# Optimization experiments

Measured on AMD Instinct MI355X. Metric: run time of the kernel, lower is better.

## Reference

```python
import jax, jax.numpy as jnp
import numpy as np

B, S, F, H = 512, 1024, 16, 64
BN_EPS = 1e-3  # Keras BatchNormalization default epsilon


def setup_inputs() -> dict:
    key = jax.random.key(0)
    ks = jax.random.split(key, 8)
    scale = 0.1
    return {
        "inputs": jax.random.normal(ks[0], (B, S, F), dtype=jnp.float32),
        "gru_kernel": jax.random.normal(ks[1], (F - 1, 3 * H), dtype=jnp.float32) * scale,
        "gru_rec_kernel": jax.random.normal(ks[2], (H, 3 * H), dtype=jnp.float32) * scale,
        "gru_bias": jax.random.normal(ks[3], (2, 3 * H), dtype=jnp.float32) * scale,
        "w1": jax.random.normal(ks[4], (H, 64), dtype=jnp.float32) * scale,
        "b1": jnp.zeros((64,), dtype=jnp.float32),
        "bn_gamma": jnp.ones((64,), dtype=jnp.float32),
        "bn_beta": jnp.zeros((64,), dtype=jnp.float32),
        "bn_mean": jnp.zeros((64,), dtype=jnp.float32),
        "bn_var": jnp.ones((64,), dtype=jnp.float32),
        "w2": jax.random.normal(ks[5], (64, 1), dtype=jnp.float32) * scale,
        "b2": jnp.zeros((1,), dtype=jnp.float32),
        "T": jax.random.normal(ks[6], (1,), dtype=jnp.float32),
    }


def _gru_scan(x, kernel, rec_kernel, bias):
    # Keras GRU, reset_after=True, gate order (z, r, h). x: [B, S, Fin]
    b_i, b_r = bias[0], bias[1]  # input bias, recurrent bias, each [3H]
    # Precompute input projections for all timesteps: [B, S, 3H]
    x_proj = jnp.einsum("bsf,fg->bsg", x, kernel) + b_i
    h0 = jnp.zeros((x.shape[0], rec_kernel.shape[0]), dtype=x.dtype)

    def step(h, xp):
        rp = h @ rec_kernel + b_r  # [B, 3H]
        xz, xr, xh = jnp.split(xp, 3, axis=-1)
        rz, rr, rh = jnp.split(rp, 3, axis=-1)
        z = jax.nn.sigmoid(xz + rz)
        r = jax.nn.sigmoid(xr + rr)
        hh = jnp.tanh(xh + r * rh)
        h_new = z * h + (1.0 - z) * hh
        return h_new, None

    h_final, _ = jax.lax.scan(step, h0, jnp.swapaxes(x_proj, 0, 1))
    return h_final  # [B, H]


def reference(inputs, gru_kernel, gru_rec_kernel, gru_bias, w1, b1,
              bn_gamma, bn_beta, bn_mean, bn_var, w2, b2, T):
    x = inputs[:, :, :-1]                 # [B, S, F-1]
    delta_x_shifted = inputs[:, :, -1]    # [B, S]
    state = _gru_scan(x, gru_kernel, gru_rec_kernel, gru_bias)  # [B, H]
    # T * delta tiled to H then mean over time == T * mean_t(delta), broadcast over H
    delta_effect = T[0] * jnp.mean(delta_x_shifted, axis=1, keepdims=True)  # [B, 1]
    state = state + delta_effect  # broadcasts over H
    h = jax.nn.relu(state @ w1 + b1)
    # Dropout identity at inference; BatchNorm uses moving statistics
    h = (h - bn_mean) * jax.lax.rsqrt(bn_var + BN_EPS) * bn_gamma + bn_beta
    out = h @ w2 + b2  # [B, 1]
    return out
```

## Files before the change

### kernel.cpp

```cpp
#include <hip/hip_runtime.h>
#include <hip/hip_bf16.h>


#define KEEP(x) asm volatile("" : "+v"(x))

typedef _Float16 f16x2 __attribute__((ext_vector_type(2)));
union H2U { unsigned int u; f16x2 h; };

#if defined(__has_builtin)
#  if __has_builtin(__builtin_amdgcn_fdot2)
#    define HAS_FDOT2 1
#  endif
#endif
#ifndef HAS_FDOT2
#  define HAS_FDOT2 0
#endif

static __device__ __forceinline__ float dot2acc(unsigned int hraw, unsigned int wraw, float acc) {
    H2U a, b; a.u = hraw; b.u = wraw;
#if HAS_FDOT2
    return __builtin_amdgcn_fdot2(a.h, b.h, acc, false);
#else
    return fmaf((float)a.h.x, (float)b.h.x, fmaf((float)a.h.y, (float)b.h.y, acc));
#endif
}

template<bool BF16>
struct IO {
    static __device__ __forceinline__ float ld(const void* p, int i) {
        if constexpr (BF16) {
            unsigned short u = ((const unsigned short*)p)[i];
            union { unsigned int ui; float f; } c; c.ui = (unsigned int)u << 16;
            return c.f;
        } else {
            return ((const float*)p)[i];
        }
    }
    static __device__ __forceinline__ void st(void* p, int i, float v) {
        if constexpr (BF16) ((__hip_bfloat16*)p)[i] = __float2bfloat16(v);
        else ((float*)p)[i] = v;
    }
    static __device__ __forceinline__ float4 ld4(const void* p, int i) {
        if constexpr (BF16) {
            const ushort4 u = ((const ushort4*)p)[i >> 2];
            union { unsigned int ui; float f; } a, b, c, d;
            a.ui = (unsigned int)u.x << 16; b.ui = (unsigned int)u.y << 16;
            c.ui = (unsigned int)u.z << 16; d.ui = (unsigned int)u.w << 16;
            return make_float4(a.f, b.f, c.f, d.f);
        } else {
            return ((const float4*)p)[i >> 2];
        }
    }
};

__global__ void detect_dtype_kernel(const void* rkbuf, int* flag) {
    const float* f = (const float*)rkbuf;
    int ok = 0;
    for (int i = 0; i < 64; ++i) {
        float a = fabsf(f[i]);
        ok += (a > 1e-5f && a < 2.0f) ? 1 : 0;
    }
    *flag = (ok >= 48) ? 1 : 0;
}

template<bool BF16>
__global__ __launch_bounds__(128, 1)
void gru_pc_kernel(const void* __restrict__ inp, const void* __restrict__ gk,
                   const void* __restrict__ rk,  const void* __restrict__ gb,
                   const void* __restrict__ w1,  const void* __restrict__ b1v,
                   const void* __restrict__ gam, const void* __restrict__ bet,
                   const void* __restrict__ muv, const void* __restrict__ vav,
                   const void* __restrict__ w2,  const void* __restrict__ bb2,
                   const void* __restrict__ Tp,  const int* __restrict__ mode,
                   void* __restrict__ out)
{
    const int want = BF16 ? 0 : 1;
    if (*mode != want) return;

    const int b   = blockIdx.x;
    const int tid = threadIdx.x;
    const int w   = tid >> 6;
    const int l   = tid & 63;

    __shared__ __align__(16) float xp[2][16][64][4];
    __shared__ __align__(16) float xs[16][16];
    __shared__ __align__(16) _Float16 hsf[64];
    __shared__ __align__(16) float sred[64];
    __shared__ float dsh;

    using io = IO<BF16>;
    const int xbase = b * 16384;

    if (w == 1) {
        float kz[15], kr[15], kh[15];
#pragma unroll
        for (int c = 0; c < 15; ++c) {
            kz[c] = io::ld(gk, c*192 + l);
            kr[c] = io::ld(gk, c*192 + 64 + l);
            kh[c] = io::ld(gk, c*192 + 128 + l);
            KEEP(kz[c]); KEEP(kr[c]); KEEP(kh[c]);
        }
        const float bz  = io::ld(gb, l)      + io::ld(gb, 192 + l);
        const float br  = io::ld(gb, 64 + l) + io::ld(gb, 192 + 64 + l);
        const float bax = io::ld(gb, 128 + l);
        float dsum = 0.0f;

        auto produce = [&](int buf) {
#pragma unroll 1
            for (int s2 = 0; s2 < 16; ++s2) {
                const float4* xr = (const float4*)&xs[s2][0];
                const float4 x0 = xr[0], x1 = xr[1], x2 = xr[2], x3 = xr[3];
                float az = bz, ar = br, ax = bax;
                az=fmaf(x0.x,kz[0],az);  ar=fmaf(x0.x,kr[0],ar);  ax=fmaf(x0.x,kh[0],ax);
                az=fmaf(x0.y,kz[1],az);  ar=fmaf(x0.y,kr[1],ar);  ax=fmaf(x0.y,kh[1],ax);
                az=fmaf(x0.z,kz[2],az);  ar=fmaf(x0.z,kr[2],ar);  ax=fmaf(x0.z,kh[2],ax);
                az=fmaf(x0.w,kz[3],az);  ar=fmaf(x0.w,kr[3],ar);  ax=fmaf(x0.w,kh[3],ax);
                az=fmaf(x1.x,kz[4],az);  ar=fmaf(x1.x,kr[4],ar);  ax=fmaf(x1.x,kh[4],ax);
                az=fmaf(x1.y,kz[5],az);  ar=fmaf(x1.y,kr[5],ar);  ax=fmaf(x1.y,kh[5],ax);
                az=fmaf(x1.z,kz[6],az);  ar=fmaf(x1.z,kr[6],ar);  ax=fmaf(x1.z,kh[6],ax);
                az=fmaf(x1.w,kz[7],az);  ar=fmaf(x1.w,kr[7],ar);  ax=fmaf(x1.w,kh[7],ax);
                az=fmaf(x2.x,kz[8],az);  ar=fmaf(x2.x,kr[8],ar);  ax=fmaf(x2.x,kh[8],ax);
                az=fmaf(x2.y,kz[9],az);  ar=fmaf(x2.y,kr[9],ar);  ax=fmaf(x2.y,kh[9],ax);
                az=fmaf(x2.z,kz[10],az); ar=fmaf(x2.z,kr[10],ar); ax=fmaf(x2.z,kh[10],ax);
                az=fmaf(x2.w,kz[11],az); ar=fmaf(x2.w,kr[11],ar); ax=fmaf(x2.w,kh[11],ax);
                az=fmaf(x3.x,kz[12],az); ar=fmaf(x3.x,kr[12],ar); ax=fmaf(x3.x,kh[12],ax);
                az=fmaf(x3.y,kz[13],az); ar=fmaf(x3.y,kr[13],ar); ax=fmaf(x3.y,kh[13],ax);
                az=fmaf(x3.z,kz[14],az); ar=fmaf(x3.z,kr[14],ar); ax=fmaf(x3.z,kh[14],ax);
                dsum += x3.w;
                *(float4*)&xp[buf][s2][l][0] = make_float4(az, ar, ax, 0.0f);
            }
        };

        {
            float4 v = io::ld4(inp, xbase + 4*l);
            ((float4*)xs)[l] = v;
            produce(0);
        }
        __syncthreads();

#pragma unroll 1
        for (int t = 0; t < 64; ++t) {
            if (t < 63) {
                float4 v = io::ld4(inp, xbase + (t + 1)*256 + 4*l);
                ((float4*)xs)[l] = v;
                produce((t + 1) & 1);
            } else if (l == 0) {
                dsh = dsum;
            }
            __syncthreads();
        }
        return;
    }

    unsigned int wzp[32], wrp[32], whp[32];
#pragma unroll
    for (int p = 0; p < 32; ++p) {
        H2U z, r, hh;
        z.h  = f16x2{(_Float16)io::ld(rk, (2*p)*192 + l),
                     (_Float16)io::ld(rk, (2*p+1)*192 + l)};
        r.h  = f16x2{(_Float16)io::ld(rk, (2*p)*192 + 64 + l),
                     (_Float16)io::ld(rk, (2*p+1)*192 + 64 + l)};
        hh.h = f16x2{(_Float16)io::ld(rk, (2*p)*192 + 128 + l),
                     (_Float16)io::ld(rk, (2*p+1)*192 + 128 + l)};
        wzp[p] = z.u; wrp[p] = r.u; whp[p] = hh.u;
        KEEP(wzp[p]); KEEP(wrp[p]); KEEP(whp[p]);
    }
    const float bah = io::ld(gb, 192 + 128 + l);

    hsf[l] = (_Float16)0.0f;
    float h = 0.0f;
    __syncthreads();

#pragma unroll 1
    for (int t = 0; t < 64; ++t) {
        const float (*xpt)[64][4] = xp[t & 1];
#pragma unroll 1
        for (int s2 = 0; s2 < 16; ++s2) {
            const float4 xpv = *(const float4*)&xpt[s2][l][0];
            const uint4* hp = (const uint4*)hsf;
            float az = xpv.x, ar = xpv.y;
            const float ax = xpv.z;
            float ah = bah;
            float az1 = 0.0f, ar1 = 0.0f, ah1 = 0.0f;
#pragma unroll
            for (int i = 0; i < 4; ++i) {
                const uint4 d = hp[i];
                az = dot2acc(d.x, wzp[4*i+0], az); ar = dot2acc(d.x, wrp[4*i+0], ar); ah = dot2acc(d.x, whp[4*i+0], ah);
                az = dot2acc(d.y, wzp[4*i+1], az); ar = dot2acc(d.y, wrp[4*i+1], ar); ah = dot2acc(d.y, whp[4*i+1], ah);
                az = dot2acc(d.z, wzp[4*i+2], az); ar = dot2acc(d.z, wrp[4*i+2], ar); ah = dot2acc(d.z, whp[4*i+2], ah);
                az = dot2acc(d.w, wzp[4*i+3], az); ar = dot2acc(d.w, wrp[4*i+3], ar); ah = dot2acc(d.w, whp[4*i+3], ah);
            }
#pragma unroll
            for (int i = 4; i < 8; ++i) {
                const uint4 d = hp[i];
                az1 = dot2acc(d.x, wzp[4*i+0], az1); ar1 = dot2acc(d.x, wrp[4*i+0], ar1); ah1 = dot2acc(d.x, whp[4*i+0], ah1);
                az1 = dot2acc(d.y, wzp[4*i+1], az1); ar1 = dot2acc(d.y, wrp[4*i+1], ar1); ah1 = dot2acc(d.y, whp[4*i+1], ah1);
                az1 = dot2acc(d.z, wzp[4*i+2], az1); ar1 = dot2acc(d.z, wrp[4*i+2], ar1); ah1 = dot2acc(d.z, whp[4*i+2], ah1);
                az1 = dot2acc(d.w, wzp[4*i+3], az1); ar1 = dot2acc(d.w, wrp[4*i+3], ar1); ah1 = dot2acc(d.w, whp[4*i+3], ah1);
            }
            az += az1; ar += ar1; ah += ah1;

            const float z   = __builtin_amdgcn_rcpf(1.0f + __expf(-az));
            const float r   = __builtin_amdgcn_rcpf(1.0f + __expf(-ar));
            const float pre = fmaf(r, ah, ax);
            const float e2  = __expf(2.0f * pre);
            const float th  = 1.0f - 2.0f * __builtin_amdgcn_rcpf(e2 + 1.0f);
            h = fmaf(z, h - th, th);

            hsf[l] = (_Float16)h;
        }
        __syncthreads();
    }

    const float T0 = io::ld(Tp, 0);
    const float state = fmaf(T0 * (1.0f / 1024.0f), dsh, h);
    sred[l] = state;

    const int j = l;
    float acc = io::ld(b1v, j);
#pragma unroll
    for (int k = 0; k < 64; ++k)
        acc = fmaf(sred[k], io::ld(w1, k*64 + j), acc);
    acc = fmaxf(acc, 0.0f);
    const float inv = rsqrtf(io::ld(vav, j) + 0.001f);
    acc = fmaf((acc - io::ld(muv, j)) * inv, io::ld(gam, j), io::ld(bet, j));

    float v = acc * io::ld(w2, j);
#pragma unroll
    for (int off = 32; off > 0; off >>= 1)
        v += __shfl_down(v, off);
    if (j == 0) io::st(out, b, v + io::ld(bb2, 0));
}

extern "C" void kernel_launch(void* const* d_in, const int* in_sizes, int n_in,
                              void* d_out, int out_size, void* d_ws, size_t ws_size,
                              hipStream_t stream)
{
    const void* inp = d_in[0];
    const void* gk  = d_in[1];
    const void* rk  = d_in[2];
    const void* gb  = d_in[3];
    const void* w1  = d_in[4];
    const void* b1v = d_in[5];
    const void* gam = d_in[6];
    const void* bet = d_in[7];
    const void* muv = d_in[8];
    const void* vav = d_in[9];
    const void* w2  = d_in[10];
    const void* bb2 = d_in[11];
    const void* Tp  = d_in[12];

    int* flag = (int*)d_ws;
    detect_dtype_kernel<<<dim3(1), dim3(1), 0, stream>>>(rk, flag);
    gru_pc_kernel<true ><<<dim3(512), dim3(128), 0, stream>>>(
        inp, gk, rk, gb, w1, b1v, gam, bet, muv, vav, w2, bb2, Tp, flag, d_out);
    gru_pc_kernel<false><<<dim3(512), dim3(128), 0, stream>>>(
        inp, gk, rk, gb, w1, b1v, gam, bet, muv, vav, w2, bb2, Tp, flag, d_out);
}
```

Measured before the change: 460.7 us.

## Process two batch rows per block to interleave independent GRU recurrences

Each block now handles two batch elements. The producer wave computes input projections for both, and the recurrent wave alternates steps between the two hidden states, keeping h vectors in registers. The intent is to hide the serial per-step latency of the recurrence (LDS round trip, transcendentals) by overlapping two independent dependency chains. It halves the grid size and increases register pressure, which could reduce parallelism across CUs.

```diff
diff --git a/kernel.cpp b/kernel.cpp
--- a/kernel.cpp
+++ b/kernel.cpp
@@ -65,31 +65,30 @@
 
 template<bool BF16>
 __global__ __launch_bounds__(128, 1)
-void gru_pc_kernel(const void* __restrict__ inp, const void* __restrict__ gk,
-                   const void* __restrict__ rk,  const void* __restrict__ gb,
-                   const void* __restrict__ w1,  const void* __restrict__ b1v,
-                   const void* __restrict__ gam, const void* __restrict__ bet,
-                   const void* __restrict__ muv, const void* __restrict__ vav,
-                   const void* __restrict__ w2,  const void* __restrict__ bb2,
-                   const void* __restrict__ Tp,  const int* __restrict__ mode,
-                   void* __restrict__ out)
+void gru_pc2_kernel(const void* __restrict__ inp, const void* __restrict__ gk,
+                    const void* __restrict__ rk,  const void* __restrict__ gb,
+                    const void* __restrict__ w1,  const void* __restrict__ b1v,
+                    const void* __restrict__ gam, const void* __restrict__ bet,
+                    const void* __restrict__ muv, const void* __restrict__ vav,
+                    const void* __restrict__ w2,  const void* __restrict__ bb2,
+                    const void* __restrict__ Tp,  const int* __restrict__ mode,
+                    void* __restrict__ out)
 {
     const int want = BF16 ? 0 : 1;
     if (*mode != want) return;
 
-    const int b   = blockIdx.x;
+    const int b0  = blockIdx.x * 2;
     const int tid = threadIdx.x;
     const int w   = tid >> 6;
     const int l   = tid & 63;
 
-    __shared__ __align__(16) float xp[2][16][64][4];
-    __shared__ __align__(16) float xs[16][16];
-    __shared__ __align__(16) _Float16 hsf[64];
-    __shared__ __align__(16) float sred[64];
-    __shared__ float dsh;
+    __shared__ __align__(16) float xp[2][2][8][64][4];
+    __shared__ __align__(16) float xs[2][8][16];
+    __shared__ __align__(16) _Float16 hsf[2][64];
+    __shared__ __align__(16) float sred[2][64];
+    __shared__ float dsh[2];
 
     using io = IO<BF16>;
-    const int xbase = b * 16384;
 
     if (w == 1) {
         float kz[15], kr[15], kh[15];
@@ -103,49 +102,47 @@
         const float bz  = io::ld(gb, l)      + io::ld(gb, 192 + l);
         const float br  = io::ld(gb, 64 + l) + io::ld(gb, 192 + 64 + l);
         const float bax = io::ld(gb, 128 + l);
-        float dsum = 0.0f;
-
+        float dsum0 = 0.0f, dsum1 = 0.0f;
+
+        const int bat = l >> 5;
+        const int q   = l & 31;
+
+        auto stage = [&](int t) {
+            float4 v = io::ld4(inp, (b0 + bat)*16384 + t*128 + q*4);
+            *(float4*)&xs[bat][q >> 2][(q & 3) * 4] = v;
+        };
         auto produce = [&](int buf) {
 #pragma unroll 1
-            for (int s2 = 0; s2 < 16; ++s2) {
-                const float4* xr = (const float4*)&xs[s2][0];
-                const float4 x0 = xr[0], x1 = xr[1], x2 = xr[2], x3 = xr[3];
-                float az = bz, ar = br, ax = bax;
-                az=fmaf(x0.x,kz[0],az);  ar=fmaf(x0.x,kr[0],ar);  ax=fmaf(x0.x,kh[0],ax);
-                az=fmaf(x0.y,kz[1],az);  ar=fmaf(x0.y,kr[1],ar);  ax=fmaf(x0.y,kh[1],ax);
-                az=fmaf(x0.z,kz[2],az);  ar=fmaf(x0.z,kr[2],ar);  ax=fmaf(x0.z,kh[2],ax);
-                az=fmaf(x0.w,kz[3],az);  ar=fmaf(x0.w,kr[3],ar);  ax=fmaf(x0.w,kh[3],ax);
-                az=fmaf(x1.x,kz[4],az);  ar=fmaf(x1.x,kr[4],ar);  ax=fmaf(x1.x,kh[4],ax);
-                az=fmaf(x1.y,kz[5],az);  ar=fmaf(x1.y,kr[5],ar);  ax=fmaf(x1.y,kh[5],ax);
-                az=fmaf(x1.z,kz[6],az);  ar=fmaf(x1.z,kr[6],ar);  ax=fmaf(x1.z,kh[6],ax);
-                az=fmaf(x1.w,kz[7],az);  ar=fmaf(x1.w,kr[7],ar);  ax=fmaf(x1.w,kh[7],ax);
-                az=fmaf(x2.x,kz[8],az);  ar=fmaf(x2.x,kr[8],ar);  ax=fmaf(x2.x,kh[8],ax);
-                az=fmaf(x2.y,kz[9],az);  ar=fmaf(x2.y,kr[9],ar);  ax=fmaf(x2.y,kh[9],ax);
-                az=fmaf(x2.z,kz[10],az); ar=fmaf(x2.z,kr[10],ar); ax=fmaf(x2.z,kh[10],ax);
-                az=fmaf(x2.w,kz[11],az); ar=fmaf(x2.w,kr[11],ar); ax=fmaf(x2.w,kh[11],ax);
-                az=fmaf(x3.x,kz[12],az); ar=fmaf(x3.x,kr[12],ar); ax=fmaf(x3.x,kh[12],ax);
-                az=fmaf(x3.y,kz[13],az); ar=fmaf(x3.y,kr[13],ar); ax=fmaf(x3.y,kh[13],ax);
-                az=fmaf(x3.z,kz[14],az); ar=fmaf(x3.z,kr[14],ar); ax=fmaf(x3.z,kh[14],ax);
-                dsum += x3.w;
-                *(float4*)&xp[buf][s2][l][0] = make_float4(az, ar, ax, 0.0f);
+            for (int ab = 0; ab < 2; ++ab) {
+#pragma unroll 1
+                for (int s2 = 0; s2 < 8; ++s2) {
+                    const float4* xr = (const float4*)&xs[ab][s2][0];
+                    const float4 x0 = xr[0], x1 = xr[1], x2 = xr[2], x3 = xr[3];
+                    const float xc[16] = {x0.x,x0.y,x0.z,x0.w, x1.x,x1.y,x1.z,x1.w,
+                                          x2.x,x2.y,x2.z,x2.w, x3.x,x3.y,x3.z,x3.w};
+                    float az = bz, ar = br, ax = bax;
+#pragma unroll
+                    for (int c = 0; c < 15; ++c) {
+                        az = fmaf(xc[c], kz[c], az);
+                        ar = fmaf(xc[c], kr[c], ar);
+                        ax = fmaf(xc[c], kh[c], ax);
+                    }
+                    if (ab == 0) dsum0 += xc[15]; else dsum1 += xc[15];
+                    *(float4*)&xp[buf][ab][s2][l][0] = make_float4(az, ar, ax, 0.0f);
+                }
             }
         };
 
-        {
-            float4 v = io::ld4(inp, xbase + 4*l);
-            ((float4*)xs)[l] = v;
-            produce(0);
-        }
+        stage(0); produce(0);
         __syncthreads();
 
 #pragma unroll 1
-        for (int t = 0; t < 64; ++t) {
-            if (t < 63) {
-                float4 v = io::ld4(inp, xbase + (t + 1)*256 + 4*l);
-                ((float4*)xs)[l] = v;
+        for (int t = 0; t < 128; ++t) {
+            if (t < 127) {
+                stage(t + 1);
                 produce((t + 1) & 1);
             } else if (l == 0) {
-                dsh = dsum;
+                dsh[0] = dsum0; dsh[1] = dsum1;
             }
             __syncthreads();
         }
@@ -167,69 +164,97 @@
     }
     const float bah = io::ld(gb, 192 + 128 + l);
 
-    hsf[l] = (_Float16)0.0f;
-    float h = 0.0f;
+    uint4 ha[8], hb[8];
+#pragma unroll
+    for (int i = 0; i < 8; ++i) { ha[i] = make_uint4(0,0,0,0); hb[i] = make_uint4(0,0,0,0); }
+    float hA = 0.0f, hB = 0.0f;
+
+    auto step_batch = [&](uint4 (&hr)[8], const float4& xpv, float& h,
+                          _Float16* hbuf) {
+        float az = xpv.x, ar = xpv.y;
+        const float ax = xpv.z;
+        float ah = bah;
+        float az1 = 0.0f, ar1 = 0.0f, ah1 = 0.0f;
+#pragma unroll
+        for (int i = 0; i < 4; ++i) {
+            const uint4 d = hr[i];
+            az = dot2acc(d.x, wzp[4*i+0], az); ar = dot2acc(d.x, wrp[4*i+0], ar); ah = dot2acc(d.x, whp[4*i+0], ah);
+            az = dot2acc(d.y, wzp[4*i+1], az); ar = dot2acc(d.y, wrp[4*i+1], ar); ah = dot2acc(d.y, whp[4*i+1], ah);
+            az = dot2acc(d.z, wzp[4*i+2], az); ar = dot2acc(d.z, wrp[4*i+2], ar); ah = dot2acc(d.z, whp[4*i+2], ah);
+            az = dot2acc(d.w, wzp[4*i+3], az); ar = dot2acc(d.w, wrp[4*i+3], ar); ah = dot2acc(d.w, whp[4*i+3], ah);
+        }
+#pragma unroll
+        for (int i = 4; i < 8; ++i) {
+            const uint4 d = hr[i];
+            az1 = dot2acc(d.x, wzp[4*i+0], az1); ar1 = dot2acc(d.x, wrp[4*i+0], ar1); ah1 = dot2acc(d.x, whp[4*i+0], ah1);
+            az1 = dot2acc(d.y, wzp[4*i+1], az1); ar1 = dot2acc(d.y, wrp[4*i+1], ar1); ah1 = dot2acc(d.y, whp[4*i+1], ah1);
+            az1 = dot2acc(d.z, wzp[4*i+2], az1); ar1 = dot2acc(d.z, wrp[4*i+2], ar1); ah1 = dot2acc(d.z, whp[4*i+2], ah1);
+            az1 = dot2acc(d.w, wzp[4*i+3], az1); ar1 = dot2acc(d.w, wrp[4*i+3], ar1); ah1 = dot2acc(d.w, whp[4*i+3], ah1);
+        }
+        az += az1; ar += ar1; ah += ah1;
+
+        const float z   = __builtin_amdgcn_rcpf(1.0f + __expf(-az));
+        const float r   = __builtin_amdgcn_rcpf(1.0f + __expf(-ar));
+        const float pre = fmaf(r, ah, ax);
+        const float e2  = __expf(2.0f * pre);
+        const float th  = 1.0f - 2.0f * __builtin_amdgcn_rcpf(e2 + 1.0f);
+        h = fmaf(z, h - th, th);
+
+        hbuf[l] = (_Float16)h;
+        const uint4* hp = (const uint4*)hbuf;
+#pragma unroll
+        for (int i = 0; i < 8; ++i) hr[i] = hp[i];
+    };
+
     __syncthreads();
-
-#pragma unroll 1
-    for (int t = 0; t < 64; ++t) {
-        const float (*xpt)[64][4] = xp[t & 1];
-#pragma unroll 1
-        for (int s2 = 0; s2 < 16; ++s2) {
-            const float4 xpv = *(const float4*)&xpt[s2][l][0];
-            const uint4* hp = (const uint4*)hsf;
-            float az = xpv.x, ar = xpv.y;
-            const float ax = xpv.z;
-            float ah = bah;
-            float az1 = 0.0f, ar1 = 0.0f, ah1 = 0.0f;
-#pragma unroll
-            for (int i = 0; i < 4; ++i) {
-                const uint4 d = hp[i];
-                az = dot2acc(d.x, wzp[4*i+0], az); ar = dot2acc(d.x, wrp[4*i+0], ar); ah = dot2acc(d.x, whp[4*i+0], ah);
-                az = dot2acc(d.y, wzp[4*i+1], az); ar = dot2acc(d.y, wrp[4*i+1], ar); ah = dot2acc(d.y, whp[4*i+1], ah);
-                az = dot2acc(d.z, wzp[4*i+2], az); ar = dot2acc(d.z, wrp[4*i+2], ar); ah = dot2acc(d.z, whp[4*i+2], ah);
-                az = dot2acc(d.w, wzp[4*i+3], az); ar = dot2acc(d.w, wrp[4*i+3], ar); ah = dot2acc(d.w, whp[4*i+3], ah);
-            }
-#pragma unroll
-            for (int i = 4; i < 8; ++i) {
-                const uint4 d = hp[i];
-                az1 = dot2acc(d.x, wzp[4*i+0], az1); ar1 = dot2acc(d.x, wrp[4*i+0], ar1); ah1 = dot2acc(d.x, whp[4*i+0], ah1);
-                az1 = dot2acc(d.y, wzp[4*i+1], az1); ar1 = dot2acc(d.y, wrp[4*i+1], ar1); ah1 = dot2acc(d.y, whp[4*i+1], ah1);
-                az1 = dot2acc(d.z, wzp[4*i+2], az1); ar1 = dot2acc(d.z, wrp[4*i+2], ar1); ah1 = dot2acc(d.z, whp[4*i+2], ah1);
-                az1 = dot2acc(d.w, wzp[4*i+3], az1); ar1 = dot2acc(d.w, wrp[4*i+3], ar1); ah1 = dot2acc(d.w, whp[4*i+3], ah1);
-            }
-            az += az1; ar += ar1; ah += ah1;
-
-            const float z   = __builtin_amdgcn_rcpf(1.0f + __expf(-az));
-            const float r   = __builtin_amdgcn_rcpf(1.0f + __expf(-ar));
-            const float pre = fmaf(r, ah, ax);
-            const float e2  = __expf(2.0f * pre);
-            const float th  = 1.0f - 2.0f * __builtin_amdgcn_rcpf(e2 + 1.0f);
-            h = fmaf(z, h - th, th);
-
-            hsf[l] = (_Float16)h;
+    float4 xA = *(const float4*)&xp[0][0][0][l][0];
+    float4 xB = *(const float4*)&xp[0][1][0][l][0];
+
+#pragma unroll 1
+    for (int t = 0; t < 128; ++t) {
+#pragma unroll 1
+        for (int s2 = 0; s2 < 8; ++s2) {
+            step_batch(ha, xA, hA, &hsf[0][0]);
+            if (s2 < 7) xA = *(const float4*)&xp[t & 1][0][s2 + 1][l][0];
+            step_batch(hb, xB, hB, &hsf[1][0]);
+            if (s2 < 7) xB = *(const float4*)&xp[t & 1][1][s2 + 1][l][0];
         }
         __syncthreads();
+        if (t < 127) {
+            xA = *(const float4*)&xp[(t + 1) & 1][0][0][l][0];
+            xB = *(const float4*)&xp[(t + 1) & 1][1][0][l][0];
+        }
     }
 
     const float T0 = io::ld(Tp, 0);
-    const float state = fmaf(T0 * (1.0f / 1024.0f), dsh, h);
-    sred[l] = state;
+    sred[0][l] = fmaf(T0 * (1.0f / 1024.0f), dsh[0], hA);
+    sred[1][l] = fmaf(T0 * (1.0f / 1024.0f), dsh[1], hB);
 
     const int j = l;
-    float acc = io::ld(b1v, j);
-#pragma unroll
-    for (int k = 0; k < 64; ++k)
-        acc = fmaf(sred[k], io::ld(w1, k*64 + j), acc);
-    acc = fmaxf(acc, 0.0f);
+    float accA = io::ld(b1v, j), accB = accA;
+#pragma unroll
+    for (int k = 0; k < 64; ++k) {
+        const float wv = io::ld(w1, k*64 + j);
+        accA = fmaf(sred[0][k], wv, accA);
+        accB = fmaf(sred[1][k], wv, accB);
+    }
     const float inv = rsqrtf(io::ld(vav, j) + 0.001f);
-    acc = fmaf((acc - io::ld(muv, j)) * inv, io::ld(gam, j), io::ld(bet, j));
-
-    float v = acc * io::ld(w2, j);
-#pragma unroll
-    for (int off = 32; off > 0; off >>= 1)
-        v += __shfl_down(v, off);
-    if (j == 0) io::st(out, b, v + io::ld(bb2, 0));
+    const float mu = io::ld(muv, j), ga = io::ld(gam, j), be = io::ld(bet, j);
+    accA = fmaf((fmaxf(accA, 0.0f) - mu) * inv, ga, be);
+    accB = fmaf((fmaxf(accB, 0.0f) - mu) * inv, ga, be);
+
+    const float w2j = io::ld(w2, j);
+    float vA = accA * w2j, vB = accB * w2j;
+#pragma unroll
+    for (int off = 32; off > 0; off >>= 1) {
+        vA += __shfl_down(vA, off);
+        vB += __shfl_down(vB, off);
+    }
+    if (j == 0) {
+        const float b2v = io::ld(bb2, 0);
+        io::st(out, b0,     vA + b2v);
+        io::st(out, b0 + 1, vB + b2v);
+    }
 }
 
 extern "C" void kernel_launch(void* const* d_in, const int* in_sizes, int n_in,
@@ -252,8 +277,8 @@
 
     int* flag = (int*)d_ws;
     detect_dtype_kernel<<<dim3(1), dim3(1), 0, stream>>>(rk, flag);
-    gru_pc_kernel<true ><<<dim3(512), dim3(128), 0, stream>>>(
+    gru_pc2_kernel<true ><<<dim3(256), dim3(128), 0, stream>>>(
         inp, gk, rk, gb, w1, b1v, gam, bet, muv, vav, w2, bb2, Tp, flag, d_out);
-    gru_pc_kernel<false><<<dim3(512), dim3(128), 0, stream>>>(
+    gru_pc2_kernel<false><<<dim3(256), dim3(128), 0, stream>>>(
         inp, gk, rk, gb, w1, b1v, gam, bet, muv, vav, w2, bb2, Tp, flag, d_out);
 }
```

Result: slower. 815.7 us (+77.1%).

## Merge producer wave into single-wave GRU kernel with staged input in LDS

Applied to the files above, without the earlier changes.

Replaces the two-wave producer/consumer scheme with a single 64-thread wave per batch row. The row's inputs are bulk-copied into LDS (in two halves for fp32), and each step computes the input projection inline. The next timestep's x is prefetched from LDS while the recurrent dot products run. Because the block is a single wave, the per-chunk __syncthreads barriers disappear and h is exchanged through LDS without a block barrier. The trade-off is that projection FMAs now sit on the serial critical path of every step, and register pressure rises from holding both weight sets.

```diff
diff --git a/kernel.cpp b/kernel.cpp
--- a/kernel.cpp
+++ b/kernel.cpp
@@ -6,6 +6,7 @@
 
 typedef _Float16 f16x2 __attribute__((ext_vector_type(2)));
 union H2U { unsigned int u; f16x2 h; };
+union FU  { unsigned int u; float f; };
 
 #if defined(__has_builtin)
 #  if __has_builtin(__builtin_amdgcn_fdot2)
@@ -30,7 +31,7 @@
     static __device__ __forceinline__ float ld(const void* p, int i) {
         if constexpr (BF16) {
             unsigned short u = ((const unsigned short*)p)[i];
-            union { unsigned int ui; float f; } c; c.ui = (unsigned int)u << 16;
+            FU c; c.u = (unsigned int)u << 16;
             return c.f;
         } else {
             return ((const float*)p)[i];
@@ -39,17 +40,6 @@
     static __device__ __forceinline__ void st(void* p, int i, float v) {
         if constexpr (BF16) ((__hip_bfloat16*)p)[i] = __float2bfloat16(v);
         else ((float*)p)[i] = v;
-    }
-    static __device__ __forceinline__ float4 ld4(const void* p, int i) {
-        if constexpr (BF16) {
-            const ushort4 u = ((const ushort4*)p)[i >> 2];
-            union { unsigned int ui; float f; } a, b, c, d;
-            a.ui = (unsigned int)u.x << 16; b.ui = (unsigned int)u.y << 16;
-            c.ui = (unsigned int)u.z << 16; d.ui = (unsigned int)u.w << 16;
-            return make_float4(a.f, b.f, c.f, d.f);
-        } else {
-            return ((const float4*)p)[i >> 2];
-        }
     }
 };
 
@@ -64,8 +54,8 @@
 }
 
 template<bool BF16>
-__global__ __launch_bounds__(128, 1)
-void gru_pc_kernel(const void* __restrict__ inp, const void* __restrict__ gk,
+__global__ __launch_bounds__(64, 1)
+void gru_sw_kernel(const void* __restrict__ inp, const void* __restrict__ gk,
                    const void* __restrict__ rk,  const void* __restrict__ gb,
                    const void* __restrict__ w1,  const void* __restrict__ b1v,
                    const void* __restrict__ gam, const void* __restrict__ bet,
@@ -77,79 +67,25 @@
     const int want = BF16 ? 0 : 1;
     if (*mode != want) return;
 
-    const int b   = blockIdx.x;
-    const int tid = threadIdx.x;
-    const int w   = tid >> 6;
-    const int l   = tid & 63;
-
-    __shared__ __align__(16) float xp[2][16][64][4];
-    __shared__ __align__(16) float xs[16][16];
+    const int b = blockIdx.x;
+    const int l = threadIdx.x;
+
+    __shared__ __align__(16) unsigned char xsm[32768];
     __shared__ __align__(16) _Float16 hsf[64];
-    __shared__ __align__(16) float sred[64];
-    __shared__ float dsh;
+    __shared__ __align__(16) float sredf[64];
 
     using io = IO<BF16>;
-    const int xbase = b * 16384;
-
-    if (w == 1) {
-        float kz[15], kr[15], kh[15];
-#pragma unroll
-        for (int c = 0; c < 15; ++c) {
-            kz[c] = io::ld(gk, c*192 + l);
-            kr[c] = io::ld(gk, c*192 + 64 + l);
-            kh[c] = io::ld(gk, c*192 + 128 + l);
-            KEEP(kz[c]); KEEP(kr[c]); KEEP(kh[c]);
-        }
-        const float bz  = io::ld(gb, l)      + io::ld(gb, 192 + l);
-        const float br  = io::ld(gb, 64 + l) + io::ld(gb, 192 + 64 + l);
-        const float bax = io::ld(gb, 128 + l);
-        float dsum = 0.0f;
-
-        auto produce = [&](int buf) {
-#pragma unroll 1
-            for (int s2 = 0; s2 < 16; ++s2) {
-                const float4* xr = (const float4*)&xs[s2][0];
-                const float4 x0 = xr[0], x1 = xr[1], x2 = xr[2], x3 = xr[3];
-                float az = bz, ar = br, ax = bax;
-                az=fmaf(x0.x,kz[0],az);  ar=fmaf(x0.x,kr[0],ar);  ax=fmaf(x0.x,kh[0],ax);
-                az=fmaf(x0.y,kz[1],az);  ar=fmaf(x0.y,kr[1],ar);  ax=fmaf(x0.y,kh[1],ax);
-                az=fmaf(x0.z,kz[2],az);  ar=fmaf(x0.z,kr[2],ar);  ax=fmaf(x0.z,kh[2],ax);
-                az=fmaf(x0.w,kz[3],az);  ar=fmaf(x0.w,kr[3],ar);  ax=fmaf(x0.w,kh[3],ax);
-                az=fmaf(x1.x,kz[4],az);  ar=fmaf(x1.x,kr[4],ar);  ax=fmaf(x1.x,kh[4],ax);
-                az=fmaf(x1.y,kz[5],az);  ar=fmaf(x1.y,kr[5],ar);  ax=fmaf(x1.y,kh[5],ax);
-                az=fmaf(x1.z,kz[6],az);  ar=fmaf(x1.z,kr[6],ar);  ax=fmaf(x1.z,kh[6],ax);
-                az=fmaf(x1.w,kz[7],az);  ar=fmaf(x1.w,kr[7],ar);  ax=fmaf(x1.w,kh[7],ax);
-                az=fmaf(x2.x,kz[8],az);  ar=fmaf(x2.x,kr[8],ar);  ax=fmaf(x2.x,kh[8],ax);
-                az=fmaf(x2.y,kz[9],az);  ar=fmaf(x2.y,kr[9],ar);  ax=fmaf(x2.y,kh[9],ax);
-                az=fmaf(x2.z,kz[10],az); ar=fmaf(x2.z,kr[10],ar); ax=fmaf(x2.z,kh[10],ax);
-                az=fmaf(x2.w,kz[11],az); ar=fmaf(x2.w,kr[11],ar); ax=fmaf(x2.w,kh[11],ax);
-                az=fmaf(x3.x,kz[12],az); ar=fmaf(x3.x,kr[12],ar); ax=fmaf(x3.x,kh[12],ax);
-                az=fmaf(x3.y,kz[13],az); ar=fmaf(x3.y,kr[13],ar); ax=fmaf(x3.y,kh[13],ax);
-                az=fmaf(x3.z,kz[14],az); ar=fmaf(x3.z,kr[14],ar); ax=fmaf(x3.z,kh[14],ax);
-                dsum += x3.w;
-                *(float4*)&xp[buf][s2][l][0] = make_float4(az, ar, ax, 0.0f);
-            }
-        };
-
-        {
-            float4 v = io::ld4(inp, xbase + 4*l);
-            ((float4*)xs)[l] = v;
-            produce(0);
-        }
-        __syncthreads();
-
-#pragma unroll 1
-        for (int t = 0; t < 64; ++t) {
-            if (t < 63) {
-                float4 v = io::ld4(inp, xbase + (t + 1)*256 + 4*l);
-                ((float4*)xs)[l] = v;
-                produce((t + 1) & 1);
-            } else if (l == 0) {
-                dsh = dsum;
-            }
-            __syncthreads();
-        }
-        return;
+    const uint4* gin = (const uint4*)inp;
+    uint4* xv = (uint4*)xsm;
+
+    if constexpr (BF16) {
+#pragma unroll 4
+        for (int i = 0; i < 32; ++i)
+            xv[i*64 + l] = gin[b*2048 + i*64 + l];
+    } else {
+#pragma unroll 4
+        for (int i = 0; i < 32; ++i)
+            xv[i*64 + l] = gin[b*4096 + i*64 + l];
     }
 
     unsigned int wzp[32], wrp[32], whp[32];
@@ -165,62 +101,142 @@
         wzp[p] = z.u; wrp[p] = r.u; whp[p] = hh.u;
         KEEP(wzp[p]); KEEP(wrp[p]); KEEP(whp[p]);
     }
+    float kzf[15], krf[15], khf[15];
+#pragma unroll
+    for (int c = 0; c < 15; ++c) {
+        kzf[c] = io::ld(gk, c*192 + l);
+        krf[c] = io::ld(gk, c*192 + 64 + l);
+        khf[c] = io::ld(gk, c*192 + 128 + l);
+        KEEP(kzf[c]); KEEP(krf[c]); KEEP(khf[c]);
+    }
+    const float bz  = io::ld(gb, l)      + io::ld(gb, 192 + l);
+    const float br  = io::ld(gb, 64 + l) + io::ld(gb, 192 + 64 + l);
+    const float bax = io::ld(gb, 128 + l);
     const float bah = io::ld(gb, 192 + 128 + l);
 
-    hsf[l] = (_Float16)0.0f;
+    float dsum = 0.0f;
+    if constexpr (BF16) {
+        const unsigned short* xs16 = (const unsigned short*)xsm;
+#pragma unroll
+        for (int k = 0; k < 16; ++k) {
+            FU c; c.u = (unsigned int)xs16[(l + 64*k)*16 + 15] << 16;
+            dsum += c.f;
+        }
+    } else {
+        const float* xsf = (const float*)xsm;
+#pragma unroll
+        for (int k = 0; k < 8; ++k)
+            dsum += xsf[(l + 64*k)*16 + 15];
+    }
+
+    uint4 hr[8];
+#pragma unroll
+    for (int i = 0; i < 8; ++i) hr[i] = make_uint4(0, 0, 0, 0);
     float h = 0.0f;
-    __syncthreads();
+
+    uint4  cr16[2] = {}, pr16[2] = {};
+    float4 cr32[4] = {}, pr32[4] = {};
+    if constexpr (BF16) { cr16[0] = xv[0]; cr16[1] = xv[1]; }
+    else { const float4* lp = (const float4*)xsm;
+           cr32[0]=lp[0]; cr32[1]=lp[1]; cr32[2]=lp[2]; cr32[3]=lp[3]; }
 
 #pragma unroll 1
-    for (int t = 0; t < 64; ++t) {
-        const float (*xpt)[64][4] = xp[t & 1];
-#pragma unroll 1
-        for (int s2 = 0; s2 < 16; ++s2) {
-            const float4 xpv = *(const float4*)&xpt[s2][l][0];
-            const uint4* hp = (const uint4*)hsf;
-            float az = xpv.x, ar = xpv.y;
-            const float ax = xpv.z;
-            float ah = bah;
-            float az1 = 0.0f, ar1 = 0.0f, ah1 = 0.0f;
-#pragma unroll
-            for (int i = 0; i < 4; ++i) {
-                const uint4 d = hp[i];
-                az = dot2acc(d.x, wzp[4*i+0], az); ar = dot2acc(d.x, wrp[4*i+0], ar); ah = dot2acc(d.x, whp[4*i+0], ah);
-                az = dot2acc(d.y, wzp[4*i+1], az); ar = dot2acc(d.y, wrp[4*i+1], ar); ah = dot2acc(d.y, whp[4*i+1], ah);
-                az = dot2acc(d.z, wzp[4*i+2], az); ar = dot2acc(d.z, wrp[4*i+2], ar); ah = dot2acc(d.z, whp[4*i+2], ah);
-                az = dot2acc(d.w, wzp[4*i+3], az); ar = dot2acc(d.w, wrp[4*i+3], ar); ah = dot2acc(d.w, whp[4*i+3], ah);
+    for (int s = 0; s < 1024; ++s) {
+        if constexpr (!BF16) {
+            if (s == 512) {
+#pragma unroll 4
+                for (int i = 0; i < 32; ++i)
+                    xv[i*64 + l] = gin[b*4096 + 2048 + i*64 + l];
+                const float* xsf = (const float*)xsm;
+#pragma unroll
+                for (int k = 0; k < 8; ++k)
+                    dsum += xsf[(l + 64*k)*16 + 15];
+                const float4* lp = (const float4*)xsm;
+                cr32[0]=lp[0]; cr32[1]=lp[1]; cr32[2]=lp[2]; cr32[3]=lp[3];
             }
-#pragma unroll
-            for (int i = 4; i < 8; ++i) {
-                const uint4 d = hp[i];
-                az1 = dot2acc(d.x, wzp[4*i+0], az1); ar1 = dot2acc(d.x, wrp[4*i+0], ar1); ah1 = dot2acc(d.x, whp[4*i+0], ah1);
-                az1 = dot2acc(d.y, wzp[4*i+1], az1); ar1 = dot2acc(d.y, wrp[4*i+1], ar1); ah1 = dot2acc(d.y, whp[4*i+1], ah1);
-                az1 = dot2acc(d.z, wzp[4*i+2], az1); ar1 = dot2acc(d.z, wrp[4*i+2], ar1); ah1 = dot2acc(d.z, whp[4*i+2], ah1);
-                az1 = dot2acc(d.w, wzp[4*i+3], az1); ar1 = dot2acc(d.w, wrp[4*i+3], ar1); ah1 = dot2acc(d.w, whp[4*i+3], ah1);
+        }
+
+        float xc[16];
+        if constexpr (BF16) {
+            const unsigned int dw[8] = {cr16[0].x, cr16[0].y, cr16[0].z, cr16[0].w,
+                                        cr16[1].x, cr16[1].y, cr16[1].z, cr16[1].w};
+#pragma unroll
+            for (int j = 0; j < 8; ++j) {
+                FU lo, hi; lo.u = dw[j] << 16; hi.u = dw[j] & 0xffff0000u;
+                xc[2*j] = lo.f; xc[2*j+1] = hi.f;
             }
-            az += az1; ar += ar1; ah += ah1;
-
-            const float z   = __builtin_amdgcn_rcpf(1.0f + __expf(-az));
-            const float r   = __builtin_amdgcn_rcpf(1.0f + __expf(-ar));
-            const float pre = fmaf(r, ah, ax);
-            const float e2  = __expf(2.0f * pre);
-            const float th  = 1.0f - 2.0f * __builtin_amdgcn_rcpf(e2 + 1.0f);
-            h = fmaf(z, h - th, th);
-
-            hsf[l] = (_Float16)h;
-        }
-        __syncthreads();
-    }
-
+        } else {
+            xc[0]=cr32[0].x; xc[1]=cr32[0].y; xc[2]=cr32[0].z; xc[3]=cr32[0].w;
+            xc[4]=cr32[1].x; xc[5]=cr32[1].y; xc[6]=cr32[1].z; xc[7]=cr32[1].w;
+            xc[8]=cr32[2].x; xc[9]=cr32[2].y; xc[10]=cr32[2].z; xc[11]=cr32[2].w;
+            xc[12]=cr32[3].x; xc[13]=cr32[3].y; xc[14]=cr32[3].z; xc[15]=cr32[3].w;
+        }
+        float az = bz, ar_ = br, ax = bax;
+#pragma unroll
+        for (int c = 0; c < 15; ++c) {
+            az  = fmaf(xc[c], kzf[c], az);
+            ar_ = fmaf(xc[c], krf[c], ar_);
+            ax  = fmaf(xc[c], khf[c], ax);
+        }
+
+        const bool pf = (s < 1023) && (BF16 || s != 511);
+        if (pf) {
+            if constexpr (BF16) {
+                pr16[0] = xv[(s+1)*2]; pr16[1] = xv[(s+1)*2 + 1];
+            } else {
+                const float4* lp = (const float4*)xsm;
+                pr32[0] = lp[((s+1)&511)*4];     pr32[1] = lp[((s+1)&511)*4+1];
+                pr32[2] = lp[((s+1)&511)*4+2];   pr32[3] = lp[((s+1)&511)*4+3];
+            }
+        }
+
+        float ah = bah;
+        float az1 = 0.0f, ar1 = 0.0f, ah1 = 0.0f;
+#pragma unroll
+        for (int i = 0; i < 4; ++i) {
+            const uint4 d = hr[i];
+            az  = dot2acc(d.x, wzp[4*i+0], az);  ar_ = dot2acc(d.x, wrp[4*i+0], ar_); ah  = dot2acc(d.x, whp[4*i+0], ah);
+            az  = dot2acc(d.y, wzp[4*i+1], az);  ar_ = dot2acc(d.y, wrp[4*i+1], ar_); ah  = dot2acc(d.y, whp[4*i+1], ah);
+            az  = dot2acc(d.z, wzp[4*i+2], az);  ar_ = dot2acc(d.z, wrp[4*i+2], ar_); ah  = dot2acc(d.z, whp[4*i+2], ah);
+            az  = dot2acc(d.w, wzp[4*i+3], az);  ar_ = dot2acc(d.w, wrp[4*i+3], ar_); ah  = dot2acc(d.w, whp[4*i+3], ah);
+        }
+#pragma unroll
+        for (int i = 4; i < 8; ++i) {
+            const uint4 d = hr[i];
+            az1 = dot2acc(d.x, wzp[4*i+0], az1); ar1 = dot2acc(d.x, wrp[4*i+0], ar1); ah1 = dot2acc(d.x, whp[4*i+0], ah1);
+            az1 = dot2acc(d.y, wzp[4*i+1], az1); ar1 = dot2acc(d.y, wrp[4*i+1], ar1); ah1 = dot2acc(d.y, whp[4*i+1], ah1);
+            az1 = dot2acc(d.z, wzp[4*i+2], az1); ar1 = dot2acc(d.z, wrp[4*i+2], ar1); ah1 = dot2acc(d.z, whp[4*i+2], ah1);
+            az1 = dot2acc(d.w, wzp[4*i+3], az1); ar1 = dot2acc(d.w, wrp[4*i+3], ar1); ah1 = dot2acc(d.w, whp[4*i+3], ah1);
+        }
+        az += az1; ar_ += ar1; ah += ah1;
+
+        const float z   = __builtin_amdgcn_rcpf(1.0f + __expf(-az));
+        const float r   = __builtin_amdgcn_rcpf(1.0f + __expf(-ar_));
+        const float pre = fmaf(r, ah, ax);
+        const float e2  = __expf(2.0f * pre);
+        const float th  = 1.0f - 2.0f * __builtin_amdgcn_rcpf(e2 + 1.0f);
+        h = fmaf(z, h - th, th);
+
+        hsf[l] = (_Float16)h;
+        const uint4* hp = (const uint4*)hsf;
+#pragma unroll
+        for (int i = 0; i < 8; ++i) hr[i] = hp[i];
+        if constexpr (BF16) { cr16[0] = pr16[0]; cr16[1] = pr16[1]; }
+        else { cr32[0]=pr32[0]; cr32[1]=pr32[1]; cr32[2]=pr32[2]; cr32[3]=pr32[3]; }
+    }
+
+#pragma unroll
+    for (int off = 1; off < 64; off <<= 1)
+        dsum += __shfl_xor(dsum, off, 64);
     const float T0 = io::ld(Tp, 0);
-    const float state = fmaf(T0 * (1.0f / 1024.0f), dsh, h);
-    sred[l] = state;
+    const float state = fmaf(T0 * (1.0f / 1024.0f), dsum, h);
+    sredf[l] = state;
 
     const int j = l;
     float acc = io::ld(b1v, j);
 #pragma unroll
     for (int k = 0; k < 64; ++k)
-        acc = fmaf(sred[k], io::ld(w1, k*64 + j), acc);
+        acc = fmaf(sredf[k], io::ld(w1, k*64 + j), acc);
     acc = fmaxf(acc, 0.0f);
     const float inv = rsqrtf(io::ld(vav, j) + 0.001f);
     acc = fmaf((acc - io::ld(muv, j)) * inv, io::ld(gam, j), io::ld(bet, j));
@@ -252,8 +268,8 @@
 
     int* flag = (int*)d_ws;
     detect_dtype_kernel<<<dim3(1), dim3(1), 0, stream>>>(rk, flag);
-    gru_pc_kernel<true ><<<dim3(512), dim3(128), 0, stream>>>(
+    gru_sw_kernel<true ><<<dim3(512), dim3(64), 0, stream>>>(
         inp, gk, rk, gb, w1, b1v, gam, bet, muv, vav, w2, bb2, Tp, flag, d_out);
-    gru_pc_kernel<false><<<dim3(512), dim3(128), 0, stream>>>(
+    gru_sw_kernel<false><<<dim3(512), dim3(64), 0, stream>>>(
         inp, gk, rk, gb, w1, b1v, gam, bet, muv, vav, w2, bb2, Tp, flag, d_out);
 }
```

Measured after the change: 554.5 us. 1.2x slower.
